# Optimization experiments

Measured on AMD Instinct MI355X. Metric: run time of the kernel, lower is better.

## Reference

```python
import jax, jax.numpy as jnp
import numpy as np

NUM_GRAPHS = 512


def setup_inputs() -> dict:
    key = jax.random.key(0)
    k1, k2, k3, k4, k5 = jax.random.split(key, 5)
    N, D = 131072, 512
    x = jax.random.normal(k1, (N, D), dtype=jnp.float32)
    graph_ptr = jnp.sort(jax.random.randint(k2, (N,), 0, NUM_GRAPHS, dtype=jnp.int64))
    # Linear(dim, dim) params (kaiming-ish scale) and query vector
    W = jax.random.normal(k3, (D, D), dtype=jnp.float32) / np.sqrt(D)
    b = jax.random.normal(k4, (D,), dtype=jnp.float32) * 0.01
    query = jax.random.normal(k5, (D,), dtype=jnp.float32)
    return {"x": x, "graph_ptr": graph_ptr, "W": W, "b": b, "query": query}


def reference(x, graph_ptr, W, b, query):
    # gate: Linear + Tanh, then score = g @ query  -> [N]
    g = jnp.tanh(x @ W.T + b)
    score = g @ query
    seg = graph_ptr.astype(jnp.int32)
    # segmented, numerically-stable softmax over nodes of each graph
    seg_max = jax.ops.segment_max(score, seg, num_segments=NUM_GRAPHS)  # [G]
    # empty segments give -inf max; they have no nodes so gather is safe
    e = jnp.exp(score - seg_max[seg])                                   # [N]
    denom = jax.ops.segment_sum(e, seg, num_segments=NUM_GRAPHS)        # [G]
    attn = e / jnp.where(denom[seg] == 0, 1.0, denom[seg])              # [N]
    # weighted scatter-sum of node features per graph -> [G, D]
    out = jax.ops.segment_sum(attn[:, None] * x, seg, num_segments=NUM_GRAPHS)
    return out
```

## Files before the change

kernel.cpp:

```cpp
#include <hip/hip_runtime.h>

typedef _Float16 f16x8 __attribute__((ext_vector_type(8)));
typedef __fp16 fp16v2 __attribute__((ext_vector_type(2)));
typedef _Float16 f16v2 __attribute__((ext_vector_type(2)));
typedef short short8 __attribute__((ext_vector_type(8)));
typedef float f32x16 __attribute__((ext_vector_type(16)));

#define DD 512
#define NG 512

typedef __attribute__((address_space(3))) void lds_void;
typedef __attribute__((address_space(1))) void glb_void;

static __device__ __forceinline__ void gload_lds16(const void* g, void* l) {
  __builtin_amdgcn_global_load_lds((const glb_void*)g, (lds_void*)l, 16, 0, 0);
}

#define WAITV(n) asm volatile("s_waitcnt vmcnt(" #n ") lgkmcnt(0)" ::: "memory")
#define MEMFENCE asm volatile("" ::: "memory")

static __device__ __forceinline__ f16v2 pk16(float a, float b) {
  fp16v2 p = __builtin_amdgcn_cvt_pkrtz(a, b);
  return __builtin_bit_cast(f16v2, p);
}

static __device__ __forceinline__ float fast_tanh(float v) {
  float e = __expf(2.0f * v);
  return 1.0f - 2.0f * __builtin_amdgcn_rcpf(e + 1.0f);
}

__global__ __launch_bounds__(256) void k_convert_w(const float* __restrict__ W,
                                                   unsigned char* __restrict__ Whl) {
  int t = blockIdx.x * 256 + threadIdx.x;
  int r512 = t >> 6, kg = t & 63;
  int ny = r512 >> 8, col = r512 & 255;
  int ct = col >> 5, c31 = col & 31;
  int kt = kg >> 1, khalf = kg & 1;
  const float* p = W + (size_t)r512 * DD + kg * 8;
  short8 h;
#pragma unroll
  for (int j = 0; j < 8; ++j) {
    _Float16 hh = (_Float16)p[j];
    h[j] = (short)__builtin_bit_cast(unsigned short, hh);
  }
  unsigned char* dst = Whl + (size_t)ny * 262144 + (size_t)kt * 8192 +
                       ct * 1024 + (khalf * 32 + c31) * 16;
  *(short8*)dst = h;
}

__global__ __launch_bounds__(256, 4) void k_gemm_score(
    const float* __restrict__ x, const unsigned char* __restrict__ Whl,
    const float* __restrict__ bias, const float* __restrict__ query,
    float* __restrict__ score_part, int N) {
  __shared__ unsigned char ldsB[3][8192];
  __shared__ unsigned char ldsA[3][4096];
  __shared__ float comb[2][64];
  const int tid = threadIdx.x;
  const int wave = tid >> 6;
  const int lane = tid & 63;
  const int l31 = lane & 31;
  const int kh = lane >> 5;
  const int rg = wave >> 1;
  const int cg = wave & 1;
  const int ny = blockIdx.x;
  const int brow0 = blockIdx.y * 64;

  const unsigned char* wsrc = Whl + (size_t)ny * 262144 +
                              (size_t)wave * 2048 + (size_t)lane * 16;

  const int c0 = wave * 64 + lane;
  const int s0c = c0 ^ ((c0 >> 3) & 7);
  const float* asrc0 = x + (size_t)(brow0 + (s0c >> 2)) * DD + (s0c & 3) * 4;

  int aoff0, aoff1;
  {
    const int row = rg * 32 + l31;
    const int u = row * 4 + 2 * kh;
    const int m = (u >> 3) & 7;
    aoff0 = (u ^ m) * 16;
    aoff1 = ((u + 1) ^ m) * 16;
  }

  f32x16 acc[4];
#pragma unroll
  for (int j = 0; j < 4; ++j)
#pragma unroll
    for (int r = 0; r < 16; ++r) acc[j][r] = 0.f;

#pragma unroll
  for (int s = 0; s < 2; ++s) {
#pragma unroll
    for (int i = 0; i < 2; ++i)
      gload_lds16(wsrc + (size_t)s * 8192 + i * 1024, &ldsB[s][wave * 2048 + i * 1024]);
    gload_lds16(asrc0 + s * 16, &ldsA[s][wave * 1024]);
    MEMFENCE;
  }

  for (int kt = 0; kt < 32; ++kt) {
    if (kt == 31) WAITV(0); else WAITV(3);
    __builtin_amdgcn_s_barrier();
    MEMFENCE;

    if (kt < 30) {
      const int s = (kt + 2) % 3;
      const unsigned char* src = wsrc + (size_t)(kt + 2) * 8192;
#pragma unroll
      for (int i = 0; i < 2; ++i)
        gload_lds16(src + i * 1024, &ldsB[s][wave * 2048 + i * 1024]);
      gload_lds16(asrc0 + (kt + 2) * 16, &ldsA[s][wave * 1024]);
    }
    MEMFENCE;

    const int slot = kt % 3;
    const unsigned char* ab = &ldsA[slot][0];
    const unsigned char* bb = &ldsB[slot][lane * 16 + cg * 4096];

    const float4 a0 = *(const float4*)(ab + aoff0);
    const float4 a1 = *(const float4*)(ab + aoff1);
    f16x8 ah;
    {
      f16v2 p;
      p = pk16(a0.x, a0.y); ah[0] = p[0]; ah[1] = p[1];
      p = pk16(a0.z, a0.w); ah[2] = p[0]; ah[3] = p[1];
      p = pk16(a1.x, a1.y); ah[4] = p[0]; ah[5] = p[1];
      p = pk16(a1.z, a1.w); ah[6] = p[0]; ah[7] = p[1];
    }

    __builtin_amdgcn_s_setprio(1);
#pragma unroll
    for (int j = 0; j < 4; ++j) {
      f16x8 bh = *(const f16x8*)(bb + j * 1024);
      acc[j] = __builtin_amdgcn_mfma_f32_32x32x16_f16(ah, bh, acc[j], 0, 0, 0);
    }
    __builtin_amdgcn_s_setprio(0);
  }

  float sp[16];
#pragma unroll
  for (int r = 0; r < 16; ++r) sp[r] = 0.f;
#pragma unroll
  for (int j = 0; j < 4; ++j) {
    const int col = ny * 256 + (cg * 4 + j) * 32 + l31;
    const float bb2 = bias[col];
    const float qq = query[col];
#pragma unroll
    for (int r = 0; r < 16; ++r)
      sp[r] += fast_tanh(acc[j][r] + bb2) * qq;
  }
  __syncthreads();
#pragma unroll
  for (int r = 0; r < 16; ++r) {
    float v = sp[r];
    v += __shfl_xor(v, 1);
    v += __shfl_xor(v, 2);
    v += __shfl_xor(v, 4);
    v += __shfl_xor(v, 8);
    v += __shfl_xor(v, 16);
    if (l31 == 0)
      comb[cg][rg * 32 + (r & 3) + 8 * (r >> 2) + 4 * kh] = v;
  }
  __syncthreads();
  if (tid < 64)
    score_part[(size_t)ny * N + brow0 + tid] = comb[0][tid] + comb[1][tid];
}

__global__ __launch_bounds__(256) void k_softmax_out(
    const float* __restrict__ x, const void* __restrict__ segp,
    const float* __restrict__ sp0, const float* __restrict__ sp1,
    float* __restrict__ out, int N) {
  const int g = blockIdx.x;
  const int tid = threadIdx.x;

  const long long probe = ((const long long*)segp)[N / 2 - 1];
  const bool is64 = ((unsigned long long)probe < (unsigned long long)NG);
  const long long* s64 = (const long long*)segp;
  const int* s32 = (const int*)segp;

  int s0, s1;
  {
    int lo = 0, hi = N;
    while (lo < hi) {
      int m = (lo + hi) >> 1;
      long long v = is64 ? s64[m] : (long long)s32[m];
      if (v < (long long)g) lo = m + 1; else hi = m;
    }
    s0 = lo;
    lo = s0; hi = N;
    while (lo < hi) {
      int m = (lo + hi) >> 1;
      long long v = is64 ? s64[m] : (long long)s32[m];
      if (v < (long long)(g + 1)) lo = m + 1; else hi = m;
    }
    s1 = lo;
  }

  __shared__ float red[4];
  __shared__ float wbuf[512];

  float lm = -INFINITY;
  for (int i = s0 + tid; i < s1; i += 256) lm = fmaxf(lm, sp0[i] + sp1[i]);
#pragma unroll
  for (int m = 1; m < 64; m <<= 1) lm = fmaxf(lm, __shfl_xor(lm, m));
  if ((tid & 63) == 0) red[tid >> 6] = lm;
  __syncthreads();
  const float mx = fmaxf(fmaxf(red[0], red[1]), fmaxf(red[2], red[3]));
  __syncthreads();

  float ls = 0.f;
  for (int i = s0 + tid; i < s1; i += 256) ls += expf(sp0[i] + sp1[i] - mx);
#pragma unroll
  for (int m = 1; m < 64; m <<= 1) ls += __shfl_xor(ls, m);
  if ((tid & 63) == 0) red[tid >> 6] = ls;
  __syncthreads();
  const float sum = red[0] + red[1] + red[2] + red[3];
  const float inv = sum > 0.f ? 1.0f / sum : 0.f;

  float a0 = 0.f, a1 = 0.f;
  const int c = tid * 2;
  for (int base = s0; base < s1; base += 512) {
    const int cnt = min(512, s1 - base);
    __syncthreads();
    for (int i = tid; i < cnt; i += 256)
      wbuf[i] = expf(sp0[base + i] + sp1[base + i] - mx) * inv;
    __syncthreads();
#pragma unroll 4
    for (int j = 0; j < cnt; ++j) {
      const float w = wbuf[j];
      const float2 xv = *(const float2*)(x + (size_t)(base + j) * DD + c);
      a0 = fmaf(w, xv.x, a0);
      a1 = fmaf(w, xv.y, a1);
    }
  }
  float* op = out + (size_t)g * DD + c;
  op[0] = a0;
  op[1] = a1;
}

extern "C" void kernel_launch(void* const* d_in, const int* in_sizes, int n_in,
                              void* d_out, int out_size, void* d_ws, size_t ws_size,
                              hipStream_t stream) {
  const float* x = (const float*)d_in[0];
  const void* seg = d_in[1];
  const float* W = (const float*)d_in[2];
  const float* b = (const float*)d_in[3];
  const float* q = (const float*)d_in[4];
  float* out = (float*)d_out;
  const int N = in_sizes[0] / DD;

  unsigned char* Whl = (unsigned char*)d_ws;
  float* sp0 = (float*)(Whl + 524288);
  float* sp1 = sp0 + N;

  k_convert_w<<<128, 256, 0, stream>>>(W, Whl);
  dim3 grid(2, N / 64);
  k_gemm_score<<<grid, 256, 0, stream>>>(x, Whl, b, q, sp0, N);
  k_softmax_out<<<NG, 256, 0, stream>>>(x, seg, sp0, sp1, out, N);
}
```

Baseline: 182.0 us.

## Enlarge GEMM-score tile to 256 rows with register-staged fp16 A and double buffering

The fused GEMM+tanh+score kernel moves from 64-row tiles with 256 threads to 256-row tiles with 512 threads (8 waves, each computing a 128x64 subtile as a 4x2 grid of MFMAs). x is now loaded into registers, converted to fp16 once and written to LDS in a swizzled layout, rather than being converted per wave on every read. K is processed in 64-wide double-buffered stages. The aim is more reuse of W and x per block and fewer redundant fp32-to-fp16 conversions, at the cost of more LDS, more registers, extra barriers per stage and fewer resident blocks.

```diff
diff --git a/kernel.cpp b/kernel.cpp
--- a/kernel.cpp
+++ b/kernel.cpp
@@ -1,6 +1,7 @@
 #include <hip/hip_runtime.h>
 
 typedef _Float16 f16x8 __attribute__((ext_vector_type(8)));
+typedef _Float16 f16x4 __attribute__((ext_vector_type(4)));
 typedef __fp16 fp16v2 __attribute__((ext_vector_type(2)));
 typedef _Float16 f16v2 __attribute__((ext_vector_type(2)));
 typedef short short8 __attribute__((ext_vector_type(8)));
@@ -16,7 +17,9 @@
   __builtin_amdgcn_global_load_lds((const glb_void*)g, (lds_void*)l, 16, 0, 0);
 }
 
-#define WAITV(n) asm volatile("s_waitcnt vmcnt(" #n ") lgkmcnt(0)" ::: "memory")
+#define WAITV(n) asm volatile("s_waitcnt vmcnt(" #n ")" ::: "memory")
+#define WAITL0 asm volatile("s_waitcnt lgkmcnt(0)" ::: "memory")
+#define BAR __builtin_amdgcn_s_barrier()
 #define MEMFENCE asm volatile("" ::: "memory")
 
 static __device__ __forceinline__ f16v2 pk16(float a, float b) {
@@ -48,120 +51,154 @@
   *(short8*)dst = h;
 }
 
-__global__ __launch_bounds__(256, 4) void k_gemm_score(
+__global__ __launch_bounds__(512, 2) void k_gemm_score(
     const float* __restrict__ x, const unsigned char* __restrict__ Whl,
     const float* __restrict__ bias, const float* __restrict__ query,
     float* __restrict__ score_part, int N) {
-  __shared__ unsigned char ldsB[3][8192];
-  __shared__ unsigned char ldsA[3][4096];
-  __shared__ float comb[2][64];
+  __shared__ unsigned char ldsA[2][32768];
+  __shared__ unsigned char ldsB[2][32768];
+  __shared__ float comb[4][256];
+
   const int tid = threadIdx.x;
   const int wave = tid >> 6;
   const int lane = tid & 63;
   const int l31 = lane & 31;
   const int kh = lane >> 5;
-  const int rg = wave >> 1;
-  const int cg = wave & 1;
+  const int wr = wave >> 2;
+  const int wc = wave & 3;
   const int ny = blockIdx.x;
-  const int brow0 = blockIdx.y * 64;
-
-  const unsigned char* wsrc = Whl + (size_t)ny * 262144 +
-                              (size_t)wave * 2048 + (size_t)lane * 16;
-
-  const int c0 = wave * 64 + lane;
-  const int s0c = c0 ^ ((c0 >> 3) & 7);
-  const float* asrc0 = x + (size_t)(brow0 + (s0c >> 2)) * DD + (s0c & 3) * 4;
-
-  int aoff0, aoff1;
-  {
-    const int row = rg * 32 + l31;
-    const int u = row * 4 + 2 * kh;
-    const int m = (u >> 3) & 7;
-    aoff0 = (u ^ m) * 16;
-    aoff1 = ((u + 1) ^ m) * 16;
-  }
-
-  f32x16 acc[4];
-#pragma unroll
-  for (int j = 0; j < 4; ++j)
-#pragma unroll
-    for (int r = 0; r < 16; ++r) acc[j][r] = 0.f;
-
-#pragma unroll
-  for (int s = 0; s < 2; ++s) {
-#pragma unroll
-    for (int i = 0; i < 2; ++i)
-      gload_lds16(wsrc + (size_t)s * 8192 + i * 1024, &ldsB[s][wave * 2048 + i * 1024]);
-    gload_lds16(asrc0 + s * 16, &ldsA[s][wave * 1024]);
-    MEMFENCE;
-  }
-
-  for (int kt = 0; kt < 32; ++kt) {
-    if (kt == 31) WAITV(0); else WAITV(3);
-    __builtin_amdgcn_s_barrier();
-    MEMFENCE;
-
-    if (kt < 30) {
-      const int s = (kt + 2) % 3;
-      const unsigned char* src = wsrc + (size_t)(kt + 2) * 8192;
-#pragma unroll
-      for (int i = 0; i < 2; ++i)
-        gload_lds16(src + i * 1024, &ldsB[s][wave * 2048 + i * 1024]);
-      gload_lds16(asrc0 + (kt + 2) * 16, &ldsA[s][wave * 1024]);
-    }
-    MEMFENCE;
-
-    const int slot = kt % 3;
-    const unsigned char* ab = &ldsA[slot][0];
-    const unsigned char* bb = &ldsB[slot][lane * 16 + cg * 4096];
-
-    const float4 a0 = *(const float4*)(ab + aoff0);
-    const float4 a1 = *(const float4*)(ab + aoff1);
-    f16x8 ah;
-    {
-      f16v2 p;
-      p = pk16(a0.x, a0.y); ah[0] = p[0]; ah[1] = p[1];
-      p = pk16(a0.z, a0.w); ah[2] = p[0]; ah[3] = p[1];
-      p = pk16(a1.x, a1.y); ah[4] = p[0]; ah[5] = p[1];
-      p = pk16(a1.z, a1.w); ah[6] = p[0]; ah[7] = p[1];
-    }
-
-    __builtin_amdgcn_s_setprio(1);
-#pragma unroll
-    for (int j = 0; j < 4; ++j) {
-      f16x8 bh = *(const f16x8*)(bb + j * 1024);
-      acc[j] = __builtin_amdgcn_mfma_f32_32x32x16_f16(ah, bh, acc[j], 0, 0, 0);
-    }
-    __builtin_amdgcn_s_setprio(0);
-  }
-
-  float sp[16];
-#pragma unroll
-  for (int r = 0; r < 16; ++r) sp[r] = 0.f;
-#pragma unroll
-  for (int j = 0; j < 4; ++j) {
-    const int col = ny * 256 + (cg * 4 + j) * 32 + l31;
+  const int brow0 = blockIdx.y * 256;
+
+  const unsigned char* wsrc = Whl + (size_t)ny * 262144 + (size_t)tid * 16;
+  const float* asrc = x + (size_t)(brow0 + (tid >> 4)) * DD + (tid & 15) * 4;
+
+  const int kc = tid & 15;
+  const int ksA = kc >> 2, hA = (kc >> 1) & 1;
+  const int cxor = (ksA << 1) | hA;
+  const int awbase = ksA * 8192 + hA * 4096 + ((tid >> 4) ^ cxor) * 16 + (kc & 1) * 8;
+
+  f32x16 acc[4][2];
+#pragma unroll
+  for (int rt = 0; rt < 4; ++rt)
+#pragma unroll
+    for (int ct = 0; ct < 2; ++ct)
+#pragma unroll
+      for (int r = 0; r < 16; ++r) acc[rt][ct][r] = 0.f;
+
+  float4 aR[8];
+
+#define BISSUE(SN, PB)                                                      \
+  do {                                                                      \
+    const unsigned char* sb_ = wsrc + (size_t)((SN) & 7) * 32768;           \
+    _Pragma("unroll")                                                       \
+    for (int i = 0; i < 4; ++i)                                             \
+      gload_lds16(sb_ + i * 8192, &ldsB[PB][tid * 16 + i * 8192]);          \
+  } while (0)
+
+#define AISSUE(SN)                                                          \
+  do {                                                                      \
+    const int sm_ = (SN) & 7;                                               \
+    _Pragma("unroll")                                                       \
+    for (int j = 0; j < 8; ++j)                                             \
+      aR[j] = *(const float4*)(asrc + (size_t)j * 32 * DD + sm_ * 64);      \
+  } while (0)
+
+#define AWRITE(PA)                                                          \
+  do {                                                                      \
+    _Pragma("unroll")                                                       \
+    for (int j = 0; j < 8; ++j) {                                           \
+      f16v2 lo_ = pk16(aR[j].x, aR[j].y);                                   \
+      f16v2 hi_ = pk16(aR[j].z, aR[j].w);                                   \
+      f16x4 v_ = {lo_[0], lo_[1], hi_[0], hi_[1]};                          \
+      *(f16x4*)(&ldsA[PA][awbase + j * 512]) = v_;                          \
+    }                                                                       \
+  } while (0)
+
+  BISSUE(0, 0);
+  MEMFENCE;
+  AISSUE(0);
+  MEMFENCE;
+  WAITV(0);
+  AWRITE(0);
+  AISSUE(1);
+  MEMFENCE;
+  WAITL0;
+  BAR;
+
+#define PHASE(S, KS)                                                        \
+  do {                                                                      \
+    const int p_ = (S) & 1;                                                 \
+    if ((KS) == 0) WAITV(8);             \
+    const unsigned char* ab_ = &ldsA[p_][(KS) * 8192 + kh * 4096 +          \
+        (wr * 128 + (l31 ^ (((KS) << 1) | kh))) * 16];                      \
+    const unsigned char* bb_ = &ldsB[p_][(KS) * 8192 + wc * 2048 + lane * 16]; \
+    f16x8 a0_ = *(const f16x8*)(ab_);                                       \
+    f16x8 a1_ = *(const f16x8*)(ab_ + 512);                                 \
+    f16x8 a2_ = *(const f16x8*)(ab_ + 1024);                                \
+    f16x8 a3_ = *(const f16x8*)(ab_ + 1536);                                \
+    f16x8 b0_ = *(const f16x8*)(bb_);                                       \
+    f16x8 b1_ = *(const f16x8*)(bb_ + 1024);                                \
+    if ((KS) == 0) { BISSUE((S) + 1, p_ ^ 1); }                             \
+    if ((KS) == 3) {                                                        \
+      WAITV(4);                         \
+      AWRITE(p_ ^ 1);                                                       \
+      AISSUE((S) + 2);                                                      \
+    }                                                                       \
+    MEMFENCE;                                                               \
+    BAR;                                                                    \
+    __builtin_amdgcn_s_setprio(1);                                          \
+    acc[0][0] = __builtin_amdgcn_mfma_f32_32x32x16_f16(a0_, b0_, acc[0][0], 0, 0, 0); \
+    acc[0][1] = __builtin_amdgcn_mfma_f32_32x32x16_f16(a0_, b1_, acc[0][1], 0, 0, 0); \
+    acc[1][0] = __builtin_amdgcn_mfma_f32_32x32x16_f16(a1_, b0_, acc[1][0], 0, 0, 0); \
+    acc[1][1] = __builtin_amdgcn_mfma_f32_32x32x16_f16(a1_, b1_, acc[1][1], 0, 0, 0); \
+    acc[2][0] = __builtin_amdgcn_mfma_f32_32x32x16_f16(a2_, b0_, acc[2][0], 0, 0, 0); \
+    acc[2][1] = __builtin_amdgcn_mfma_f32_32x32x16_f16(a2_, b1_, acc[2][1], 0, 0, 0); \
+    acc[3][0] = __builtin_amdgcn_mfma_f32_32x32x16_f16(a3_, b0_, acc[3][0], 0, 0, 0); \
+    acc[3][1] = __builtin_amdgcn_mfma_f32_32x32x16_f16(a3_, b1_, acc[3][1], 0, 0, 0); \
+    __builtin_amdgcn_s_setprio(0);                                          \
+    if ((KS) == 3) WAITL0;  \
+    MEMFENCE;                                                               \
+    BAR;                                                                    \
+  } while (0)
+
+#define STEP(S) do { PHASE(S, 0); PHASE(S, 1); PHASE(S, 2); PHASE(S, 3); } while (0)
+
+  STEP(0); STEP(1); STEP(2); STEP(3);
+  STEP(4); STEP(5); STEP(6); STEP(7);
+
+  float sp[4][16];
+#pragma unroll
+  for (int rt = 0; rt < 4; ++rt)
+#pragma unroll
+    for (int r = 0; r < 16; ++r) sp[rt][r] = 0.f;
+#pragma unroll
+  for (int ct = 0; ct < 2; ++ct) {
+    const int col = ny * 256 + (wc * 2 + ct) * 32 + l31;
     const float bb2 = bias[col];
     const float qq = query[col];
 #pragma unroll
-    for (int r = 0; r < 16; ++r)
-      sp[r] += fast_tanh(acc[j][r] + bb2) * qq;
-  }
-  __syncthreads();
-#pragma unroll
-  for (int r = 0; r < 16; ++r) {
-    float v = sp[r];
-    v += __shfl_xor(v, 1);
-    v += __shfl_xor(v, 2);
-    v += __shfl_xor(v, 4);
-    v += __shfl_xor(v, 8);
-    v += __shfl_xor(v, 16);
-    if (l31 == 0)
-      comb[cg][rg * 32 + (r & 3) + 8 * (r >> 2) + 4 * kh] = v;
-  }
-  __syncthreads();
-  if (tid < 64)
-    score_part[(size_t)ny * N + brow0 + tid] = comb[0][tid] + comb[1][tid];
+    for (int rt = 0; rt < 4; ++rt)
+#pragma unroll
+      for (int r = 0; r < 16; ++r)
+        sp[rt][r] += fast_tanh(acc[rt][ct][r] + bb2) * qq;
+  }
+#pragma unroll
+  for (int rt = 0; rt < 4; ++rt)
+#pragma unroll
+    for (int r = 0; r < 16; ++r) {
+      float v = sp[rt][r];
+      v += __shfl_xor(v, 1);
+      v += __shfl_xor(v, 2);
+      v += __shfl_xor(v, 4);
+      v += __shfl_xor(v, 8);
+      v += __shfl_xor(v, 16);
+      if (l31 == 0)
+        comb[wc][wr * 128 + rt * 32 + (r & 3) + 8 * (r >> 2) + 4 * kh] = v;
+    }
+  __syncthreads();
+  if (tid < 256)
+    score_part[(size_t)ny * N + brow0 + tid] =
+        comb[0][tid] + comb[1][tid] + comb[2][tid] + comb[3][tid];
 }
 
 __global__ __launch_bounds__(256) void k_softmax_out(
@@ -252,7 +289,7 @@
   float* sp1 = sp0 + N;
 
   k_convert_w<<<128, 256, 0, stream>>>(W, Whl);
-  dim3 grid(2, N / 64);
-  k_gemm_score<<<grid, 256, 0, stream>>>(x, Whl, b, q, sp0, N);
+  dim3 grid(2, N / 256);
+  k_gemm_score<<<grid, 512, 0, stream>>>(x, Whl, b, q, sp0, N);
   k_softmax_out<<<NG, 256, 0, stream>>>(x, seg, sp0, sp1, out, N);
 }
```

Result: slower. 217.3 us (+19.4%).
